# Kernel optimization log

Hardware: AMD Instinct MI355X
Metric: run time of the kernel (lower is better)

## Reference

```python
import jax, jax.numpy as jnp
import numpy as np

B = 16; IMG = 127; INC = 64; GROUP = 1; STRIDE = 2; PAD = 1; KS = 3
G = INC // GROUP            # number of ScannCore blocks
S = KS * KS                 # patch_size (attention dim) = 9
SPN = (IMG + 2 * PAD - KS) // STRIDE + 1   # 64
PN = SPN * SPN              # patch_num = 4096
L = GROUP * PN              # sequence length per core


def setup_inputs() -> dict:
    key = jax.random.key(0)
    ks = jax.random.split(key, 9)
    sc = 1.0 / np.sqrt(S)
    x = jax.random.normal(ks[0], (B, INC, IMG, IMG), jnp.float32)
    Wq = jax.random.uniform(ks[1], (G, S, S), jnp.float32, -sc, sc)
    bq = jax.random.uniform(ks[2], (G, S), jnp.float32, -sc, sc)
    Wk = jax.random.uniform(ks[3], (G, S, S), jnp.float32, -sc, sc)
    bk = jax.random.uniform(ks[4], (G, S), jnp.float32, -sc, sc)
    Wv = jax.random.uniform(ks[5], (G, S, S), jnp.float32, -sc, sc)
    bv = jax.random.uniform(ks[6], (G, S), jnp.float32, -sc, sc)
    Wo = jax.random.uniform(ks[7], (G, S, 1), jnp.float32, -sc, sc)
    bo = jax.random.uniform(ks[8], (G, 1), jnp.float32, -sc, sc)
    return dict(x=x, Wq=Wq, bq=bq, Wk=Wk, bk=bk, Wv=Wv, bv=bv, Wo=Wo, bo=bo)


def reference(x, Wq, bq, Wk, bk, Wv, bv, Wo, bo):
    # F.unfold equivalent: [B, INC*S, SPN, SPN] with feature dim ordered (C, kh, kw)
    patches = jax.lax.conv_general_dilated_patches(
        x, (KS, KS), (STRIDE, STRIDE), [(PAD, PAD), (PAD, PAD)])
    t = patches.reshape(B, INC, S, PN)
    # split channels into G groups of GROUP, move patch axis before patch-pixel axis
    t = t.reshape(B, G, GROUP, S, PN).transpose(0, 1, 2, 4, 3).reshape(B, G, L, S)
    # batched tiny single-head attention across all G cores at once
    Q = jnp.einsum('bgls,gst->bglt', t, Wq) + bq[None, :, None, :]
    Km = jnp.einsum('bgls,gst->bglt', t, Wk) + bk[None, :, None, :]
    V = jnp.einsum('bgls,gst->bglt', t, Wv) + bv[None, :, None, :]
    # energy = K^T @ Q over the L axis -> [B, G, S, S]
    energy = jnp.einsum('bgls,bglt->bgst', Km, Q)
    attn = jax.nn.softmax(energy, axis=-1)   # dropout is identity in eval
    # (attn @ V^T)^T -> [B, G, L, S]
    a = jnp.einsum('bgst,bglt->bgls', attn, V)
    out = jnp.einsum('bgls,gso->bglo', a, Wo) + bo[None, :, None, :]  # [B,G,L,1]
    # faithful reshape/permute of original: [B, spn, spn, group] -> [B, group, spn, spn]
    out = out.reshape(B, G, SPN, SPN, GROUP).transpose(0, 1, 4, 2, 3)
    return out.reshape(B, INC, SPN, SPN)
```

## Files before the change

### kernel.cpp

```cpp
#include <hip/hip_runtime.h>
#include <math.h>

#define NB       16
#define IMG      127
#define PLANE    (IMG * IMG)
#define PN       4096
#define NTHREADS 512
#define PPT      8
#define NROW     (2 * PPT + 1)

#define GLOBAL_AS __attribute__((address_space(1)))
#define LDS_AS    __attribute__((address_space(3)))

__device__ __forceinline__ constexpr int symidx(int p, int q) {
    return p * 9 - (p * (p - 1)) / 2 + (q - p);
}

__device__ __forceinline__ float dpp_wave_shr1(float v) {
    return __builtin_bit_cast(float, __builtin_amdgcn_update_dpp(
        0, __builtin_bit_cast(int, v), 0x138, 0xf, 0xf, true));
}

__device__ __forceinline__ float wave_reduce_full(float v) {
#define DPP_ADD(ctrl)                                                          \
    v += __builtin_bit_cast(float, __builtin_amdgcn_update_dpp(                \
             0, __builtin_bit_cast(int, v), (ctrl), 0xf, 0xf, true))
    DPP_ADD(0x111);
    DPP_ADD(0x112);
    DPP_ADD(0x114);
    DPP_ADD(0x118);
    DPP_ADD(0x142);
    DPP_ADD(0x143);
#undef DPP_ADD
    return v;
}

#define XLANE_FENCE() __builtin_amdgcn_wave_barrier()

__global__ void __launch_bounds__(NTHREADS, 2)
scann_fused(const float* __restrict__ x,
            const float* __restrict__ Wq, const float* __restrict__ bq,
            const float* __restrict__ Wk, const float* __restrict__ bk,
            const float* __restrict__ Wv, const float* __restrict__ bv,
            const float* __restrict__ Wo, const float* __restrict__ bo,
            float* __restrict__ out)
{
    __shared__ float plane[PLANE];
    __shared__ float red[8 * 54];
    __shared__ float Msh[45];
    __shared__ float msh[9];
    __shared__ float MW[81];
    __shared__ float Wq_s[81], Wk_s[81], Wv_s[81];
    __shared__ float bq_s[9], bk_s[9], bv_s[9], Wo_s[9];
    __shared__ float en[81], at[81], wt[9], u_s[9];
    __shared__ float c_s, bo_sh;

    const int bg  = blockIdx.x;
    const int g   = bg & 63;
    const int tid = threadIdx.x;
    const int ow  = tid & 63;
    const int wv  = tid >> 6;
    const int oh0 = wv * PPT;

    const float* __restrict__ xp = x + (size_t)bg * PLANE;

    const int a0 = (4 - (bg & 3)) & 3;
    if (tid < a0) plane[tid] = xp[tid];
    #pragma unroll
    for (int j = 0; j < 7; ++j) {
        __builtin_amdgcn_global_load_lds(
            (const GLOBAL_AS void*)(xp + a0 + (j * NTHREADS + tid) * 4),
            (LDS_AS void*)(&plane[a0 + (j * NTHREADS + wv * 64) * 4]), 16, 0, 0);
    }
    {
        const int base = a0 + 7 * NTHREADS * 4;
        const int cnt  = PLANE - base;
        for (int i = tid; i < cnt; i += NTHREADS)
            plane[base + i] = xp[base + i];
    }

    if (tid < 81) {
        Wq_s[tid] = Wq[g * 81 + tid];
        Wk_s[tid] = Wk[g * 81 + tid];
        Wv_s[tid] = Wv[g * 81 + tid];
    } else if (tid >= 128 && tid < 137) {
        const int i = tid - 128;
        bq_s[i] = bq[g * 9 + i];
        bk_s[i] = bk[g * 9 + i];
        bv_s[i] = bv[g * 9 + i];
        Wo_s[i] = Wo[g * 9 + i];
    } else if (tid == 192) {
        bo_sh = bo[g];
    }
    __syncthreads();

    const bool c2  = (ow < 63);
    const int  ih0 = oh0 * 2 - 1;

    float e0[NROW], e1[NROW];
    #pragma unroll
    for (int r = 0; r < NROW; ++r) {
        const int ih = ih0 + r;
        float a = 0.f, b = 0.f;
        if ((unsigned)ih < (unsigned)IMG) {
            const int wa = ih * IMG + 2 * ow;
            a = plane[wa];
            if (c2) b = plane[wa + 1];
        }
        e0[r] = a; e1[r] = b;
    }

    float acc[45], mm[9];
    #pragma unroll
    for (int i = 0; i < 45; ++i) acc[i] = 0.f;
    #pragma unroll
    for (int i = 0; i < 9; ++i)  mm[i] = 0.f;

    #pragma unroll
    for (int k = 0; k < PPT; ++k) {
        float v[9];
        #pragma unroll
        for (int r = 0; r < 3; ++r) {
            const int rr = 2 * k + r;
            v[3 * r + 0] = dpp_wave_shr1(e1[rr]);
            v[3 * r + 1] = e0[rr];
            v[3 * r + 2] = e1[rr];
        }
        int idx = 0;
        #pragma unroll
        for (int p = 0; p < 9; ++p) {
            mm[p] += v[p];
            #pragma unroll
            for (int q = p; q < 9; ++q)
                acc[idx++] += v[p] * v[q];
        }
    }

    #pragma unroll
    for (int i = 0; i < 45; ++i) acc[i] = wave_reduce_full(acc[i]);
    #pragma unroll
    for (int i = 0; i < 9; ++i)  mm[i] = wave_reduce_full(mm[i]);
    if (ow == 63) {
        #pragma unroll
        for (int i = 0; i < 45; ++i) red[wv * 54 + i]      = acc[i];
        #pragma unroll
        for (int i = 0; i < 9; ++i)  red[wv * 54 + 45 + i] = mm[i];
    }
    __syncthreads();

    if (wv == 0) {
        const int lane = ow;
        if (lane < 54) {
            float s = 0.f;
            #pragma unroll
            for (int w = 0; w < 8; ++w) s += red[w * 54 + lane];
            if (lane < 45) Msh[lane]      = s;
            else           msh[lane - 45] = s;
        }
        XLANE_FENCE();
        #pragma unroll
        for (int r = 0; r < 2; ++r) {
            const int e = lane + r * 64;
            if (e < 81) {
                const int p = e / 9, t = e % 9;
                float a2 = 0.f;
                #pragma unroll
                for (int q = 0; q < 9; ++q) {
                    const int a_ = p < q ? p : q, b_ = p < q ? q : p;
                    a2 += Msh[symidx(a_, b_)] * Wq_s[q * 9 + t];
                }
                MW[e] = a2;
            }
        }
        XLANE_FENCE();
        #pragma unroll
        for (int r = 0; r < 2; ++r) {
            const int e = lane + r * 64;
            if (e < 81) {
                const int s = e / 9, t = e % 9;
                float km = 0.f, qm = 0.f, a2 = 0.f;
                #pragma unroll
                for (int p = 0; p < 9; ++p) {
                    km += Wk_s[p * 9 + s] * msh[p];
                    qm += Wq_s[p * 9 + t] * msh[p];
                    a2 += Wk_s[p * 9 + s] * MW[p * 9 + t];
                }
                en[e] = a2 + (float)PN * bk_s[s] * bq_s[t] + km * bq_s[t] + bk_s[s] * qm;
            }
        }
        XLANE_FENCE();
        if (lane < 9) {
            const int s = lane;
            float mx = en[s * 9];
            #pragma unroll
            for (int t = 1; t < 9; ++t) mx = fmaxf(mx, en[s * 9 + t]);
            float ex[9], sum = 0.f;
            #pragma unroll
            for (int t = 0; t < 9; ++t) { ex[t] = expf(en[s * 9 + t] - mx); sum += ex[t]; }
            const float inv = 1.f / sum;
            #pragma unroll
            for (int t = 0; t < 9; ++t) at[s * 9 + t] = ex[t] * inv;
        }
        XLANE_FENCE();
        if (lane < 9) {
            const int t = lane;
            float w = 0.f;
            #pragma unroll
            for (int s = 0; s < 9; ++s) w += at[s * 9 + t] * Wo_s[s];
            wt[t] = w;
        }
        XLANE_FENCE();
        if (lane < 9) {
            const int p = lane;
            float uu = 0.f;
            #pragma unroll
            for (int t = 0; t < 9; ++t) uu += Wv_s[p * 9 + t] * wt[t];
            u_s[p] = uu;
        }
        if (lane == 12) {
            float cc = bo_sh;
            #pragma unroll
            for (int t = 0; t < 9; ++t) cc += bv_s[t] * wt[t];
            c_s = cc;
        }
    }
    __syncthreads();

    float ur[9];
    #pragma unroll
    for (int i = 0; i < 9; ++i) ur[i] = u_s[i];
    const float cc = c_s;
    float* __restrict__ op = out + (size_t)bg * PN;

    #pragma unroll
    for (int k = 0; k < PPT; ++k) {
        float o = cc;
        #pragma unroll
        for (int r = 0; r < 3; ++r) {
            const int rr = 2 * k + r;
            o += dpp_wave_shr1(e1[rr]) * ur[3 * r + 0];
            o += e0[rr]                * ur[3 * r + 1];
            o += e1[rr]                * ur[3 * r + 2];
        }
        op[(oh0 + k) * 64 + ow] = o;
    }
}

extern "C" void kernel_launch(void* const* d_in, const int* in_sizes, int n_in,
                              void* d_out, int out_size, void* d_ws, size_t ws_size,
                              hipStream_t stream) {
    (void)in_sizes; (void)n_in; (void)d_ws; (void)ws_size; (void)out_size;
    const float* x  = (const float*)d_in[0];
    const float* Wq = (const float*)d_in[1];
    const float* bq = (const float*)d_in[2];
    const float* Wk = (const float*)d_in[3];
    const float* bk = (const float*)d_in[4];
    const float* Wv = (const float*)d_in[5];
    const float* bv = (const float*)d_in[6];
    const float* Wo = (const float*)d_in[7];
    const float* bo = (const float*)d_in[8];
    float* out = (float*)d_out;

    dim3 grid(NB * 64), block(NTHREADS);
    hipLaunchKernelGGL(scann_fused, grid, block, 0, stream,
                       x, Wq, bq, Wk, bk, Wv, bv, Wo, bo, out);
}
```

Before: 45.76 us.

## Split fused kernel into gram, tiny-attention, and output kernels

Replaces the single fused kernel, which staged each 127x127 plane in LDS, with three launches. The first computes per-plane Gram sums directly from global memory, the second derives the folded output weights in 64-thread blocks, and the third re-reads x to produce the output with a rolling register window. The split removes the 64KB LDS plane and the serial single-wave tail inside the big kernel, which should allow higher occupancy. In exchange x is read twice, two extra launches are added, and intermediates make a round trip through the workspace.

```diff
diff --git a/kernel.cpp b/kernel.cpp
--- a/kernel.cpp
+++ b/kernel.cpp
@@ -5,12 +5,10 @@
 #define IMG      127
 #define PLANE    (IMG * IMG)
 #define PN       4096
-#define NTHREADS 512
 #define PPT      8
 #define NROW     (2 * PPT + 1)
 
-#define GLOBAL_AS __attribute__((address_space(1)))
-#define LDS_AS    __attribute__((address_space(3)))
+#define WS_UC    (1024 * 64)
 
 __device__ __forceinline__ constexpr int symidx(int p, int q) {
     return p * 9 - (p * (p - 1)) / 2 + (q - p);
@@ -37,63 +35,18 @@
 
 #define XLANE_FENCE() __builtin_amdgcn_wave_barrier()
 
-__global__ void __launch_bounds__(NTHREADS, 2)
-scann_fused(const float* __restrict__ x,
-            const float* __restrict__ Wq, const float* __restrict__ bq,
-            const float* __restrict__ Wk, const float* __restrict__ bk,
-            const float* __restrict__ Wv, const float* __restrict__ bv,
-            const float* __restrict__ Wo, const float* __restrict__ bo,
-            float* __restrict__ out)
+__global__ void __launch_bounds__(512, 2)
+k1_gram(const float* __restrict__ x, float* __restrict__ wsp)
 {
-    __shared__ float plane[PLANE];
     __shared__ float red[8 * 54];
-    __shared__ float Msh[45];
-    __shared__ float msh[9];
-    __shared__ float MW[81];
-    __shared__ float Wq_s[81], Wk_s[81], Wv_s[81];
-    __shared__ float bq_s[9], bk_s[9], bv_s[9], Wo_s[9];
-    __shared__ float en[81], at[81], wt[9], u_s[9];
-    __shared__ float c_s, bo_sh;
 
     const int bg  = blockIdx.x;
-    const int g   = bg & 63;
     const int tid = threadIdx.x;
     const int ow  = tid & 63;
     const int wv  = tid >> 6;
     const int oh0 = wv * PPT;
 
     const float* __restrict__ xp = x + (size_t)bg * PLANE;
-
-    const int a0 = (4 - (bg & 3)) & 3;
-    if (tid < a0) plane[tid] = xp[tid];
-    #pragma unroll
-    for (int j = 0; j < 7; ++j) {
-        __builtin_amdgcn_global_load_lds(
-            (const GLOBAL_AS void*)(xp + a0 + (j * NTHREADS + tid) * 4),
-            (LDS_AS void*)(&plane[a0 + (j * NTHREADS + wv * 64) * 4]), 16, 0, 0);
-    }
-    {
-        const int base = a0 + 7 * NTHREADS * 4;
-        const int cnt  = PLANE - base;
-        for (int i = tid; i < cnt; i += NTHREADS)
-            plane[base + i] = xp[base + i];
-    }
-
-    if (tid < 81) {
-        Wq_s[tid] = Wq[g * 81 + tid];
-        Wk_s[tid] = Wk[g * 81 + tid];
-        Wv_s[tid] = Wv[g * 81 + tid];
-    } else if (tid >= 128 && tid < 137) {
-        const int i = tid - 128;
-        bq_s[i] = bq[g * 9 + i];
-        bk_s[i] = bk[g * 9 + i];
-        bv_s[i] = bv[g * 9 + i];
-        Wo_s[i] = Wo[g * 9 + i];
-    } else if (tid == 192) {
-        bo_sh = bo[g];
-    }
-    __syncthreads();
-
     const bool c2  = (ow < 63);
     const int  ih0 = oh0 * 2 - 1;
 
@@ -103,9 +56,9 @@
         const int ih = ih0 + r;
         float a = 0.f, b = 0.f;
         if ((unsigned)ih < (unsigned)IMG) {
-            const int wa = ih * IMG + 2 * ow;
-            a = plane[wa];
-            if (c2) b = plane[wa + 1];
+            const float* __restrict__ rp = xp + ih * IMG + 2 * ow;
+            a = rp[0];
+            if (c2) b = rp[1];
         }
         e0[r] = a; e1[r] = b;
     }
@@ -148,108 +101,161 @@
     }
     __syncthreads();
 
-    if (wv == 0) {
-        const int lane = ow;
-        if (lane < 54) {
-            float s = 0.f;
+    if (tid < 54) {
+        float s = 0.f;
+        #pragma unroll
+        for (int w = 0; w < 8; ++w) s += red[w * 54 + tid];
+        wsp[bg * 64 + tid] = s;
+    }
+}
+
+__global__ void __launch_bounds__(64, 4)
+k2_tiny(const float* __restrict__ wsp, float* __restrict__ wuc,
+        const float* __restrict__ Wq, const float* __restrict__ bq,
+        const float* __restrict__ Wk, const float* __restrict__ bk,
+        const float* __restrict__ Wv, const float* __restrict__ bv,
+        const float* __restrict__ Wo, const float* __restrict__ bo)
+{
+    __shared__ float Msh[45], msh[9], MW[81], en[81], at[81], wt[9];
+
+    const int bg   = blockIdx.x;
+    const int g    = bg & 63;
+    const int lane = threadIdx.x;
+
+    const float* __restrict__ Wqg = Wq + g * 81;
+    const float* __restrict__ Wkg = Wk + g * 81;
+    const float* __restrict__ Wvg = Wv + g * 81;
+
+    if (lane < 54) {
+        const float s = wsp[bg * 64 + lane];
+        if (lane < 45) Msh[lane]      = s;
+        else           msh[lane - 45] = s;
+    }
+    XLANE_FENCE();
+    #pragma unroll
+    for (int r = 0; r < 2; ++r) {
+        const int e = lane + r * 64;
+        if (e < 81) {
+            const int p = e / 9, t = e % 9;
+            float a2 = 0.f;
             #pragma unroll
-            for (int w = 0; w < 8; ++w) s += red[w * 54 + lane];
-            if (lane < 45) Msh[lane]      = s;
-            else           msh[lane - 45] = s;
-        }
-        XLANE_FENCE();
-        #pragma unroll
-        for (int r = 0; r < 2; ++r) {
-            const int e = lane + r * 64;
-            if (e < 81) {
-                const int p = e / 9, t = e % 9;
-                float a2 = 0.f;
-                #pragma unroll
-                for (int q = 0; q < 9; ++q) {
-                    const int a_ = p < q ? p : q, b_ = p < q ? q : p;
-                    a2 += Msh[symidx(a_, b_)] * Wq_s[q * 9 + t];
-                }
-                MW[e] = a2;
+            for (int q = 0; q < 9; ++q) {
+                const int a_ = p < q ? p : q, b_ = p < q ? q : p;
+                a2 += Msh[symidx(a_, b_)] * Wqg[q * 9 + t];
             }
-        }
-        XLANE_FENCE();
-        #pragma unroll
-        for (int r = 0; r < 2; ++r) {
-            const int e = lane + r * 64;
-            if (e < 81) {
-                const int s = e / 9, t = e % 9;
-                float km = 0.f, qm = 0.f, a2 = 0.f;
-                #pragma unroll
-                for (int p = 0; p < 9; ++p) {
-                    km += Wk_s[p * 9 + s] * msh[p];
-                    qm += Wq_s[p * 9 + t] * msh[p];
-                    a2 += Wk_s[p * 9 + s] * MW[p * 9 + t];
-                }
-                en[e] = a2 + (float)PN * bk_s[s] * bq_s[t] + km * bq_s[t] + bk_s[s] * qm;
+            MW[e] = a2;
+        }
+    }
+    XLANE_FENCE();
+    #pragma unroll
+    for (int r = 0; r < 2; ++r) {
+        const int e = lane + r * 64;
+        if (e < 81) {
+            const int s = e / 9, t = e % 9;
+            float km = 0.f, qm = 0.f, a2 = 0.f;
+            #pragma unroll
+            for (int p = 0; p < 9; ++p) {
+                km += Wkg[p * 9 + s] * msh[p];
+                qm += Wqg[p * 9 + t] * msh[p];
+                a2 += Wkg[p * 9 + s] * MW[p * 9 + t];
             }
-        }
-        XLANE_FENCE();
-        if (lane < 9) {
-            const int s = lane;
-            float mx = en[s * 9];
-            #pragma unroll
-            for (int t = 1; t < 9; ++t) mx = fmaxf(mx, en[s * 9 + t]);
-            float ex[9], sum = 0.f;
-            #pragma unroll
-            for (int t = 0; t < 9; ++t) { ex[t] = expf(en[s * 9 + t] - mx); sum += ex[t]; }
-            const float inv = 1.f / sum;
-            #pragma unroll
-            for (int t = 0; t < 9; ++t) at[s * 9 + t] = ex[t] * inv;
-        }
-        XLANE_FENCE();
-        if (lane < 9) {
-            const int t = lane;
-            float w = 0.f;
-            #pragma unroll
-            for (int s = 0; s < 9; ++s) w += at[s * 9 + t] * Wo_s[s];
-            wt[t] = w;
-        }
-        XLANE_FENCE();
-        if (lane < 9) {
-            const int p = lane;
-            float uu = 0.f;
-            #pragma unroll
-            for (int t = 0; t < 9; ++t) uu += Wv_s[p * 9 + t] * wt[t];
-            u_s[p] = uu;
-        }
-        if (lane == 12) {
-            float cc = bo_sh;
-            #pragma unroll
-            for (int t = 0; t < 9; ++t) cc += bv_s[t] * wt[t];
-            c_s = cc;
-        }
-    }
-    __syncthreads();
+            en[e] = a2 + (float)PN * bk[g * 9 + s] * bq[g * 9 + t]
+                  + km * bq[g * 9 + t] + bk[g * 9 + s] * qm;
+        }
+    }
+    XLANE_FENCE();
+    if (lane < 9) {
+        const int s = lane;
+        float mx = en[s * 9];
+        #pragma unroll
+        for (int t = 1; t < 9; ++t) mx = fmaxf(mx, en[s * 9 + t]);
+        float ex[9], sum = 0.f;
+        #pragma unroll
+        for (int t = 0; t < 9; ++t) { ex[t] = expf(en[s * 9 + t] - mx); sum += ex[t]; }
+        const float inv = 1.f / sum;
+        #pragma unroll
+        for (int t = 0; t < 9; ++t) at[s * 9 + t] = ex[t] * inv;
+    }
+    XLANE_FENCE();
+    if (lane < 9) {
+        const int t = lane;
+        float w = 0.f;
+        #pragma unroll
+        for (int s = 0; s < 9; ++s) w += at[s * 9 + t] * Wo[g * 9 + s];
+        wt[t] = w;
+    }
+    XLANE_FENCE();
+    if (lane < 9) {
+        const int p = lane;
+        float uu = 0.f;
+        #pragma unroll
+        for (int t = 0; t < 9; ++t) uu += Wvg[p * 9 + t] * wt[t];
+        wuc[bg * 16 + p] = uu;
+    }
+    if (lane == 12) {
+        float cc = bo[g];
+        #pragma unroll
+        for (int t = 0; t < 9; ++t) cc += bv[g * 9 + t] * wt[t];
+        wuc[bg * 16 + 9] = cc;
+    }
+}
+
+__global__ void __launch_bounds__(512, 4)
+k3_out(const float* __restrict__ x, const float* __restrict__ wuc,
+       float* __restrict__ out)
+{
+    const int bg  = blockIdx.x;
+    const int tid = threadIdx.x;
+    const int ow  = tid & 63;
+    const int wv  = tid >> 6;
+    const int oh0 = wv * PPT;
+
+    const float* __restrict__ xp = x + (size_t)bg * PLANE;
+    const float* __restrict__ up = wuc + bg * 16;
 
     float ur[9];
     #pragma unroll
-    for (int i = 0; i < 9; ++i) ur[i] = u_s[i];
-    const float cc = c_s;
+    for (int i = 0; i < 9; ++i) ur[i] = up[i];
+    const float cc = up[9];
+
+    const bool c2  = (ow < 63);
+    const int  ih0 = oh0 * 2 - 1;
     float* __restrict__ op = out + (size_t)bg * PN;
 
+    float a0, b0, a1, b1, a2, b2;
+#define LOAD_PAIR(A, B, ihv)                                                   \
+    {                                                                          \
+        const int ih_ = (ihv);                                                 \
+        A = 0.f; B = 0.f;                                                      \
+        if ((unsigned)ih_ < (unsigned)IMG) {                                   \
+            const float* __restrict__ rp_ = xp + ih_ * IMG + 2 * ow;           \
+            A = rp_[0];                                                        \
+            if (c2) B = rp_[1];                                                \
+        }                                                                      \
+    }
+    LOAD_PAIR(a0, b0, ih0 + 0);
+    LOAD_PAIR(a1, b1, ih0 + 1);
+    LOAD_PAIR(a2, b2, ih0 + 2);
     #pragma unroll
     for (int k = 0; k < PPT; ++k) {
         float o = cc;
-        #pragma unroll
-        for (int r = 0; r < 3; ++r) {
-            const int rr = 2 * k + r;
-            o += dpp_wave_shr1(e1[rr]) * ur[3 * r + 0];
-            o += e0[rr]                * ur[3 * r + 1];
-            o += e1[rr]                * ur[3 * r + 2];
-        }
+        o += dpp_wave_shr1(b0) * ur[0]; o += a0 * ur[1]; o += b0 * ur[2];
+        o += dpp_wave_shr1(b1) * ur[3]; o += a1 * ur[4]; o += b1 * ur[5];
+        o += dpp_wave_shr1(b2) * ur[6]; o += a2 * ur[7]; o += b2 * ur[8];
         op[(oh0 + k) * 64 + ow] = o;
-    }
+        if (k < PPT - 1) {
+            a0 = a2; b0 = b2;
+            LOAD_PAIR(a1, b1, ih0 + 2 * k + 3);
+            LOAD_PAIR(a2, b2, ih0 + 2 * k + 4);
+        }
+    }
+#undef LOAD_PAIR
 }
 
 extern "C" void kernel_launch(void* const* d_in, const int* in_sizes, int n_in,
                               void* d_out, int out_size, void* d_ws, size_t ws_size,
                               hipStream_t stream) {
-    (void)in_sizes; (void)n_in; (void)d_ws; (void)ws_size; (void)out_size;
+    (void)in_sizes; (void)n_in; (void)ws_size; (void)out_size;
     const float* x  = (const float*)d_in[0];
     const float* Wq = (const float*)d_in[1];
     const float* bq = (const float*)d_in[2];
@@ -260,8 +266,11 @@
     const float* Wo = (const float*)d_in[7];
     const float* bo = (const float*)d_in[8];
     float* out = (float*)d_out;
-
-    dim3 grid(NB * 64), block(NTHREADS);
-    hipLaunchKernelGGL(scann_fused, grid, block, 0, stream,
-                       x, Wq, bq, Wk, bk, Wv, bv, Wo, bo, out);
-}
+    float* wsp = (float*)d_ws;
+    float* wuc = wsp + WS_UC;
+
+    hipLaunchKernelGGL(k1_gram, dim3(NB * 64), dim3(512), 0, stream, x, wsp);
+    hipLaunchKernelGGL(k2_tiny, dim3(NB * 64), dim3(64), 0, stream,
+                       wsp, wuc, Wq, bq, Wk, bk, Wv, bv, Wo, bo);
+    hipLaunchKernelGGL(k3_out, dim3(NB * 64), dim3(512), 0, stream, x, wuc, out);
+}
```

Measured after the change: 47.98 us. +4.9%, slower.
